# Kernel tuning notes

Measured on AMD Instinct MI355X. Metric: run time of the kernel, lower is better.

Reference implementation:

```python
import jax, jax.numpy as jnp
import numpy as np

B = 16384
C = 512          # mean candidate count per sample
T = B * C        # total flat logits length (static)


def _seg_ce(logits, counts, gt, valid, B):
    """Segmented cross-entropy over variable-length candidate sets.
    logits: [T] flat concatenated logits; counts: [B] segment lengths (sum == T);
    gt: [B] target index within each segment; valid: [B] bool mask.
    Returns (mean loss over valid samples, n_correct, n_valid)."""
    Ttot = logits.shape[0]
    offsets = jnp.cumsum(counts) - counts                       # [B] start of each segment
    seg = jnp.repeat(jnp.arange(B), counts, total_repeat_length=Ttot)  # [T] segment ids
    segmax = jax.ops.segment_max(logits, seg, num_segments=B)   # [B]
    ex = jnp.exp(logits - segmax[seg])
    Z = jax.ops.segment_sum(ex, seg, num_segments=B)            # [B]
    lse = jnp.log(Z) + segmax                                   # [B] logsumexp per segment
    # target logit: clamp position for safety; invalid rows are masked out anyway
    pos = offsets + jnp.clip(gt, 0, jnp.maximum(counts - 1, 0))
    ce = lse - logits[pos]                                      # [B]
    in_range = (gt >= 0) & (gt < counts)
    vmask = (counts > 0) & in_range & valid
    n_valid = vmask.sum()
    loss = jnp.where(vmask, ce, 0.0).sum() / jnp.maximum(n_valid, 1)
    # argmax within each segment (first occurrence, matching torch.argmax)
    local = jnp.arange(Ttot) - offsets[seg]
    is_max = logits == segmax[seg]
    arg = jax.ops.segment_min(jnp.where(is_max, local, Ttot), seg, num_segments=B)
    n_correct = (vmask & (arg == gt)).sum()
    return loss, n_correct, n_valid


def setup_inputs() -> dict:
    key = jax.random.key(0)
    ks = jax.random.split(key, 8)
    # counts alternate C+32 / C-32 so sum == B*C exactly (static T)
    counts = jnp.where(jnp.arange(B) % 2 == 0, C + 32, C - 32).astype(jnp.int32)
    sys_logits = jax.random.normal(ks[0], (T,), dtype=jnp.float32)
    bar_logits = jax.random.normal(ks[1], (T,), dtype=jnp.float32)
    gt_system_idx = jax.random.randint(ks[2], (B,), 0, C - 32).astype(jnp.int32)
    gt_bar_in_sys = jax.random.randint(ks[3], (B,), 0, C - 32).astype(jnp.int32)
    note_positions = jax.random.uniform(ks[4], (B,), dtype=jnp.float32)
    gt_note_position = jax.random.uniform(ks[5], (B,), dtype=jnp.float32)
    gt_valid = jax.random.bernoulli(ks[6], 0.97, (B,))
    return {
        'sys_logits': sys_logits, 'sys_counts': counts,
        'bar_logits': bar_logits, 'bar_counts': counts,
        'note_positions': note_positions,
        'gt_system_idx': gt_system_idx, 'gt_bar_in_sys': gt_bar_in_sys,
        'gt_note_position': gt_note_position, 'gt_valid': gt_valid,
        'log_var_sys': jnp.zeros((), jnp.float32),
        'log_var_bar': jnp.zeros((), jnp.float32),
        'log_var_note': jnp.zeros((), jnp.float32),
    }


def reference(sys_logits, sys_counts, bar_logits, bar_counts, note_positions,
              gt_system_idx, gt_bar_in_sys, gt_note_position, gt_valid,
              log_var_sys, log_var_bar, log_var_note):
    Bn = gt_system_idx.shape[0]
    sys_loss, sys_correct, n_valid = _seg_ce(sys_logits, sys_counts, gt_system_idx, gt_valid, Bn)
    bar_loss, bar_correct, n_valid_bar = _seg_ce(bar_logits, bar_counts, gt_bar_in_sys, gt_valid, Bn)
    # note position MSE over valid samples (bar_valid == gt_valid here)
    m = gt_valid
    nsel = m.sum()
    sq = jnp.where(m, (note_positions - gt_note_position) ** 2, 0.0)
    note_loss = jnp.where(nsel > 0, sq.sum() / jnp.maximum(nsel, 1), 0.0)
    prec_sys = jnp.exp(-log_var_sys)
    prec_bar = jnp.exp(-log_var_bar)
    prec_note = jnp.exp(-log_var_note)
    loss = (0.5 * prec_sys * sys_loss + 0.5 * log_var_sys
            + 0.5 * prec_bar * bar_loss + 0.5 * log_var_bar
            + 0.5 * prec_note * note_loss + 0.5 * log_var_note)
    sys_acc = sys_correct / jnp.maximum(n_valid, 1)
    bar_acc = bar_correct / jnp.maximum(n_valid_bar, 1)
    return (loss, sys_loss, bar_loss, note_loss, sys_acc, bar_acc,
            prec_sys, prec_bar, prec_note)
```

## Files before the change

### kernel.cpp

```cpp
#include <hip/hip_runtime.h>
#include <math.h>

#define SCAN_BLOCKS 256
#define NOTE_SQ   256
#define NOTE_CNT  512
#define DESC_BASE 1024

__device__ __forceinline__ bool is_valid(const void* gv, int flag, int i) {
  if (flag == 0) return ((const int*)gv)[i] != 0;
  if (flag == 1) return ((const unsigned char*)gv)[i] != 0;
  return ((const float*)gv)[i] != 0.0f;
}

__global__ __launch_bounds__(256)
void uwl_scan_desc(const int* __restrict__ c_sys, const int* __restrict__ c_bar,
                   const int* __restrict__ gt_sys, const int* __restrict__ gt_bar,
                   const void* __restrict__ gv,
                   const float* __restrict__ npos, const float* __restrict__ gnp,
                   int B, int* __restrict__ wsI, float* __restrict__ wsF) {
  const int blk = blockIdx.x;
  const int tid = threadIdx.x;
  const int lane = tid & 63;
  const int wid = tid >> 6;
  __shared__ int s_flag;
  __shared__ int sS[4], sB[4];
  const int chunk = (B + SCAN_BLOCKS - 1) / SCAN_BLOCKS;
  const int start0 = blk * chunk;
  const int start = (start0 < B) ? start0 : B;
  const int end = (start0 + chunk < B) ? start0 + chunk : B;
  if (tid < 64) {
    int nw = B / 4; if (nw > 64) nw = 64; if (nw < 1) nw = 1;
    const unsigned int x = (tid < nw) ? ((const unsigned int*)gv)[tid] : 0u;
    const bool all01 = __all(x <= 1u);
    const bool allf = __all(x == 0u || x == 0x3F800000u);
    if (tid == 0) s_flag = all01 ? 0 : (allf ? 2 : 1);
  }
  if (blk == 0) {
    if (tid >= 1 && tid <= 8) wsI[tid * 16] = 0;
    if (tid == 9) wsI[144] = 0;
  }
  int bs = 0, bb = 0;
  {
    const int s4 = start >> 2;
    const int4* cs4 = (const int4*)c_sys;
    const int4* cb4 = (const int4*)c_bar;
    for (int j = tid; j < s4; j += 256) {
      const int4 a = cs4[j]; bs += a.x + a.y + a.z + a.w;
      const int4 b = cb4[j]; bb += b.x + b.y + b.z + b.w;
    }
    if (tid < (start & 3)) {
      bs += c_sys[(s4 << 2) + tid];
      bb += c_bar[(s4 << 2) + tid];
    }
  }
#pragma unroll
  for (int d = 1; d < 64; d <<= 1) {
    bs += __shfl_xor(bs, d, 64);
    bb += __shfl_xor(bb, d, 64);
  }
  if (lane == 0) { sS[wid] = bs; sB[wid] = bb; }
  __syncthreads();
  const int flag = s_flag;
  if (wid == 0) {
    int carry1 = sS[0] + sS[1] + sS[2] + sS[3];
    int carry2 = sB[0] + sB[1] + sB[2] + sB[3];
    int4* descS = (int4*)(wsI + DESC_BASE);
    int4* descB = descS + B;
    for (int base = start; base < end; base += 64) {
      const int idx = base + lane;
      const bool ok = idx < end;
      const int x1 = ok ? c_sys[idx] : 0;
      const int x2 = ok ? c_bar[idx] : 0;
      int o1 = x1, o2 = x2;
#pragma unroll
      for (int d = 1; d < 64; d <<= 1) {
        const int v1 = __shfl_up(o1, d, 64);
        const int v2 = __shfl_up(o2, d, 64);
        if (lane >= d) { o1 += v1; o2 += v2; }
      }
      if (ok) {
        const int g1 = gt_sys[idx], g2 = gt_bar[idx];
        const bool v = is_valid(gv, flag, idx);
        descS[idx] = make_int4(carry1 + o1 - x1, x1, g1,
                               (x1 > 0 && g1 >= 0 && g1 < x1 && v) ? 1 : 0);
        descB[idx] = make_int4(carry2 + o2 - x2, x2, g2,
                               (x2 > 0 && g2 >= 0 && g2 < x2 && v) ? 1 : 0);
      }
      carry1 += __shfl(o1, 63, 64);
      carry2 += __shfl(o2, 63, 64);
    }
  } else if (wid == 1) {
    float sq = 0.f; int cnt = 0;
    for (int i = start + lane; i < end; i += 64) {
      if (is_valid(gv, flag, i)) {
        const float d = npos[i] - gnp[i];
        sq += d * d; cnt += 1;
      }
    }
#pragma unroll
    for (int d = 1; d < 64; d <<= 1) {
      sq += __shfl_xor(sq, d, 64);
      cnt += __shfl_xor(cnt, d, 64);
    }
    if (lane == 0) {
      wsF[NOTE_SQ + blk] = sq;
      wsI[NOTE_CNT + blk] = cnt;
    }
  }
}

__global__ __launch_bounds__(256)
void uwl_ce_kernel(const float* __restrict__ sys_lg, const float* __restrict__ bar_lg,
                   int B, int* __restrict__ wsI, float* __restrict__ wsF) {
  const int lane = threadIdx.x & 63;
  const int wid = threadIdx.x >> 6;
  const int wstep = (int)(gridDim.x << 2);
  for (int wave0 = (int)(blockIdx.x << 2) + wid; wave0 < 2 * B; wave0 += wstep) {
    const int wave = __builtin_amdgcn_readfirstlane(wave0);
    const int4 d4 = ((const int4*)(wsI + DESC_BASE))[wave];
    const float* lg = (wave < B) ? sys_lg : bar_lg;
    const int off_i = d4.x, count = d4.y, gt = d4.z, vld = d4.w;
    const long long off = off_i;

    float m = -INFINITY;
    float s = 0.f;
    float tl = 0.f;
    const bool regpath = (count >= 4) && (count <= 576) &&
                         ((off_i & 3) == 0) && ((count & 3) == 0);
    if (regpath) {
      const float4* p = (const float4*)(lg + off);
      const int emax = (count >> 2) - 1;
      float vals[8];
#pragma unroll
      for (int k = 0; k < 2; ++k) {
        const int e4 = (k << 6) + lane;
        const int ec = (e4 > emax) ? emax : e4;
        const float4 v = p[ec];
        const bool live = (e4 <= emax);
        vals[4 * k]     = live ? v.x : -INFINITY;
        vals[4 * k + 1] = live ? v.y : -INFINITY;
        vals[4 * k + 2] = live ? v.z : -INFINITY;
        vals[4 * k + 3] = live ? v.w : -INFINITY;
      }
      const int ti = 512 + lane;
      const int tic = (ti < count) ? ti : (count - 1);
      const float tvr = lg[off + tic];
      const float tv = (ti < count) ? tvr : -INFINITY;
#pragma unroll
      for (int k = 0; k < 8; ++k) m = fmaxf(m, vals[k]);
      m = fmaxf(m, tv);
#pragma unroll
      for (int k = 0; k < 8; ++k) s += __expf(vals[k]);
      s += __expf(tv);
      const int gts = vld ? gt : 0;
      float pick;
      int srclane;
      if (gts < 512) {
        const int q = ((gts >> 8) << 2) | (gts & 3);
        pick = vals[0];
#pragma unroll
        for (int i = 1; i < 8; ++i) pick = (i == q) ? vals[i] : pick;
        srclane = (gts >> 2) & 63;
      } else {
        pick = tv;
        srclane = gts - 512;
      }
      tl = __shfl(pick, srclane, 64);
    } else {
      for (int i = lane; i < count; i += 64) {
        const float v = lg[off + i];
        m = fmaxf(m, v);
        s += __expf(v);
      }
      if (vld) {
        const float t0 = (lane == 0) ? lg[off + gt] : 0.f;
        tl = __shfl(t0, 0, 64);
      }
    }
#pragma unroll
    for (int d = 1; d < 64; d <<= 1) {
      s += __shfl_xor(s, d, 64);
      m = fmaxf(m, __shfl_xor(m, d, 64));
    }
    if (lane == 0) {
      float ce = 0.f, code = 0.f;
      if (vld) {
        ce = __logf(s) - tl;
        code = (tl == m) ? 3.f : 1.f;
      }
      ((float2*)(wsF + DESC_BASE + 8 * B))[wave] = make_float2(ce, code);
    }
  }
}

__global__ __launch_bounds__(256)
void uwl_reduce_kernel(const float* __restrict__ lvs_p, const float* __restrict__ lvb_p,
                       const float* __restrict__ lvn_p,
                       int B, int* wsI, float* wsF, float* __restrict__ out) {
  const float4* pw4 = (const float4*)(wsF + DESC_BASE + 8 * B);
  float ces = 0.f, ceb = 0.f;
  int nvs = 0, cs = 0, nvb = 0, cb = 0;
  const int stride = gridDim.x * blockDim.x;
  for (int j = blockIdx.x * blockDim.x + threadIdx.x; j < B; j += stride) {
    const float4 v = pw4[j];
    const int e0 = 2 * j, e1 = 2 * j + 1;
    const int c0 = (int)v.y, c1 = (int)v.w;
    if (e0 < B) { ces += v.x; nvs += c0 & 1; cs += c0 >> 1; }
    else        { ceb += v.x; nvb += c0 & 1; cb += c0 >> 1; }
    if (e1 < B) { ces += v.z; nvs += c1 & 1; cs += c1 >> 1; }
    else        { ceb += v.z; nvb += c1 & 1; cb += c1 >> 1; }
  }
  float sq = 0.f; int cnt = 0;
  if (blockIdx.x == 0 && threadIdx.x < SCAN_BLOCKS) {
    sq = wsF[NOTE_SQ + threadIdx.x];
    cnt = wsI[NOTE_CNT + threadIdx.x];
  }
#pragma unroll
  for (int d = 1; d < 64; d <<= 1) {
    ces += __shfl_xor(ces, d, 64);
    ceb += __shfl_xor(ceb, d, 64);
    nvs += __shfl_xor(nvs, d, 64);
    cs  += __shfl_xor(cs,  d, 64);
    nvb += __shfl_xor(nvb, d, 64);
    cb  += __shfl_xor(cb,  d, 64);
    sq  += __shfl_xor(sq,  d, 64);
    cnt += __shfl_xor(cnt, d, 64);
  }
  if ((threadIdx.x & 63) == 0) {
    atomicAdd(&wsI[16], nvs);
    atomicAdd(&wsI[32], cs);
    atomicAdd(&wsF[48], ces);
    atomicAdd(&wsI[64], nvb);
    atomicAdd(&wsI[80], cb);
    atomicAdd(&wsF[96], ceb);
    atomicAdd(&wsI[112], cnt);
    atomicAdd(&wsF[128], sq);
  }
  __syncthreads();
  if (threadIdx.x == 0) {
    __threadfence();
    const int t = atomicAdd(&wsI[144], 1);
    if (t == (int)gridDim.x - 1) {
      __threadfence();
      const int fnvs = atomicAdd(&wsI[16], 0);
      const int fcs  = atomicAdd(&wsI[32], 0);
      const int fnvb = atomicAdd(&wsI[64], 0);
      const int fcb  = atomicAdd(&wsI[80], 0);
      const int fnn  = atomicAdd(&wsI[112], 0);
      const float fces = atomicAdd(&wsF[48], 0.f);
      const float fceb = atomicAdd(&wsF[96], 0.f);
      const float fsq  = atomicAdd(&wsF[128], 0.f);
      const float sys_loss = fces / (float)(fnvs > 1 ? fnvs : 1);
      const float bar_loss = fceb / (float)(fnvb > 1 ? fnvb : 1);
      const float note_loss = (fnn > 0) ? fsq / (float)fnn : 0.f;
      const float lvs = lvs_p[0], lvb = lvb_p[0], lvn = lvn_p[0];
      const float ps = expf(-lvs), pb = expf(-lvb), pn = expf(-lvn);
      out[0] = 0.5f * (ps * sys_loss + lvs + pb * bar_loss + lvb + pn * note_loss + lvn);
      out[1] = sys_loss;
      out[2] = bar_loss;
      out[3] = note_loss;
      out[4] = (float)fcs / (float)(fnvs > 1 ? fnvs : 1);
      out[5] = (float)fcb / (float)(fnvb > 1 ? fnvb : 1);
      out[6] = ps;
      out[7] = pb;
      out[8] = pn;
    }
  }
}

extern "C" void kernel_launch(void* const* d_in, const int* in_sizes, int n_in,
                              void* d_out, int out_size, void* d_ws, size_t ws_size,
                              hipStream_t stream) {
  const float* sys_lg = (const float*)d_in[0];
  const int*   c_sys  = (const int*)d_in[1];
  const float* bar_lg = (const float*)d_in[2];
  const int*   c_bar  = (const int*)d_in[3];
  const float* npos   = (const float*)d_in[4];
  const int*   gt_sys = (const int*)d_in[5];
  const int*   gt_bar = (const int*)d_in[6];
  const float* gnp    = (const float*)d_in[7];
  const void*  gv     = d_in[8];
  const float* lvs    = (const float*)d_in[9];
  const float* lvb    = (const float*)d_in[10];
  const float* lvn    = (const float*)d_in[11];
  const int B = in_sizes[1];

  int*   wsI = (int*)d_ws;
  float* wsF = (float*)d_ws;

  uwl_scan_desc<<<SCAN_BLOCKS, 256, 0, stream>>>(c_sys, c_bar, gt_sys, gt_bar, gv,
                                                 npos, gnp, B, wsI, wsF);

  const long long nwaveslots = ((long long)(2 * B) + 3) / 4;
  int nblocks = (int)((nwaveslots < 2048) ? nwaveslots : 2048);
  if (nblocks < 1) nblocks = 1;
  uwl_ce_kernel<<<nblocks, 256, 0, stream>>>(sys_lg, bar_lg, B, wsI, wsF);

  uwl_reduce_kernel<<<64, 256, 0, stream>>>(lvs, lvb, lvn, B, wsI, wsF, (float*)d_out);
}
```

Measured before the change: 131.6 us.

## Fuse descriptor scan and segment CE into one kernel with per-block prefix recompute

Merges the count-scan/descriptor kernel and the cross-entropy kernel into one kernel. Each block now owns 16 segments, recomputes its global offset by summing all preceding counts, and keeps the descriptors in shared memory. Per-block partial sums go to the workspace and a single-block final kernel reduces them, replacing the atomic last-block reduction. Valid and correct counts are packed into one int using 16-bit fields. This removes a launch and the descriptor round trip through global memory, but every block redundantly re-reads the count prefix, which adds a lot of L2 traffic. The 16-bit packing also limits the batch size.

```diff
diff --git a/kernel.cpp b/kernel.cpp
--- a/kernel.cpp
+++ b/kernel.cpp
@@ -1,10 +1,7 @@
 #include <hip/hip_runtime.h>
 #include <math.h>
 
-#define SCAN_BLOCKS 256
-#define NOTE_SQ   256
-#define NOTE_CNT  512
-#define DESC_BASE 1024
+#define SEG_PER_BLOCK 16
 
 __device__ __forceinline__ bool is_valid(const void* gv, int flag, int i) {
   if (flag == 0) return ((const int*)gv)[i] != 0;
@@ -13,21 +10,24 @@
 }
 
 __global__ __launch_bounds__(256)
-void uwl_scan_desc(const int* __restrict__ c_sys, const int* __restrict__ c_bar,
-                   const int* __restrict__ gt_sys, const int* __restrict__ gt_bar,
-                   const void* __restrict__ gv,
-                   const float* __restrict__ npos, const float* __restrict__ gnp,
-                   int B, int* __restrict__ wsI, float* __restrict__ wsF) {
-  const int blk = blockIdx.x;
+void uwl_fused(const float* __restrict__ sys_lg, const float* __restrict__ bar_lg,
+               const int* __restrict__ c_sys, const int* __restrict__ c_bar,
+               const int* __restrict__ gt_sys, const int* __restrict__ gt_bar,
+               const void* __restrict__ gv,
+               const float* __restrict__ npos, const float* __restrict__ gnp,
+               int B, int NB, int* __restrict__ wsI, float* __restrict__ wsF) {
+  const int b = blockIdx.x;
   const int tid = threadIdx.x;
   const int lane = tid & 63;
   const int wid = tid >> 6;
+  const int g0 = b * SEG_PER_BLOCK;
   __shared__ int s_flag;
-  __shared__ int sS[4], sB[4];
-  const int chunk = (B + SCAN_BLOCKS - 1) / SCAN_BLOCKS;
-  const int start0 = blk * chunk;
-  const int start = (start0 < B) ? start0 : B;
-  const int end = (start0 + chunk < B) ? start0 + chunk : B;
+  __shared__ int sOff[SEG_PER_BLOCK], sCnt[SEG_PER_BLOCK];
+  __shared__ int sGt[SEG_PER_BLOCK], sVld[SEG_PER_BLOCK];
+  __shared__ int sB1[4], sB2[4];
+  __shared__ float sCe[4], sCb[4];
+  __shared__ int sCo[4], sCob[4];
+
   if (tid < 64) {
     int nw = B / 4; if (nw > 64) nw = 64; if (nw < 1) nw = 1;
     const unsigned int x = (tid < nw) ? ((const unsigned int*)gv)[tid] : 0u;
@@ -35,63 +35,62 @@
     const bool allf = __all(x == 0u || x == 0x3F800000u);
     if (tid == 0) s_flag = all01 ? 0 : (allf ? 2 : 1);
   }
-  if (blk == 0) {
-    if (tid >= 1 && tid <= 8) wsI[tid * 16] = 0;
-    if (tid == 9) wsI[144] = 0;
-  }
+
+  const int e1 = (g0 < B) ? g0 : 0;
+  int e2 = g0 - B; if (e2 < 0) e2 = 0; if (e2 > B) e2 = B;
   int bs = 0, bb = 0;
   {
-    const int s4 = start >> 2;
-    const int4* cs4 = (const int4*)c_sys;
-    const int4* cb4 = (const int4*)c_bar;
-    for (int j = tid; j < s4; j += 256) {
-      const int4 a = cs4[j]; bs += a.x + a.y + a.z + a.w;
-      const int4 b = cb4[j]; bb += b.x + b.y + b.z + b.w;
-    }
-    if (tid < (start & 3)) {
-      bs += c_sys[(s4 << 2) + tid];
-      bb += c_bar[(s4 << 2) + tid];
-    }
+    const int s4 = e1 >> 2;
+    const int4* c4 = (const int4*)c_sys;
+    for (int j = tid; j < s4; j += 256) { const int4 a = c4[j]; bs += a.x + a.y + a.z + a.w; }
+    if (tid < (e1 & 3)) bs += c_sys[(s4 << 2) + tid];
+  }
+  {
+    const int s4 = e2 >> 2;
+    const int4* c4 = (const int4*)c_bar;
+    for (int j = tid; j < s4; j += 256) { const int4 a = c4[j]; bb += a.x + a.y + a.z + a.w; }
+    if (tid < (e2 & 3)) bb += c_bar[(s4 << 2) + tid];
   }
 #pragma unroll
   for (int d = 1; d < 64; d <<= 1) {
     bs += __shfl_xor(bs, d, 64);
     bb += __shfl_xor(bb, d, 64);
   }
-  if (lane == 0) { sS[wid] = bs; sB[wid] = bb; }
+  if (lane == 0) { sB1[wid] = bs; sB2[wid] = bb; }
   __syncthreads();
   const int flag = s_flag;
+
   if (wid == 0) {
-    int carry1 = sS[0] + sS[1] + sS[2] + sS[3];
-    int carry2 = sB[0] + sB[1] + sB[2] + sB[3];
-    int4* descS = (int4*)(wsI + DESC_BASE);
-    int4* descB = descS + B;
-    for (int base = start; base < end; base += 64) {
-      const int idx = base + lane;
-      const bool ok = idx < end;
-      const int x1 = ok ? c_sys[idx] : 0;
-      const int x2 = ok ? c_bar[idx] : 0;
-      int o1 = x1, o2 = x2;
-#pragma unroll
-      for (int d = 1; d < 64; d <<= 1) {
-        const int v1 = __shfl_up(o1, d, 64);
-        const int v2 = __shfl_up(o2, d, 64);
-        if (lane >= d) { o1 += v1; o2 += v2; }
-      }
-      if (ok) {
-        const int g1 = gt_sys[idx], g2 = gt_bar[idx];
-        const bool v = is_valid(gv, flag, idx);
-        descS[idx] = make_int4(carry1 + o1 - x1, x1, g1,
-                               (x1 > 0 && g1 >= 0 && g1 < x1 && v) ? 1 : 0);
-        descB[idx] = make_int4(carry2 + o2 - x2, x2, g2,
-                               (x2 > 0 && g2 >= 0 && g2 < x2 && v) ? 1 : 0);
-      }
-      carry1 += __shfl(o1, 63, 64);
-      carry2 += __shfl(o2, 63, 64);
+    const int base1 = sB1[0] + sB1[1] + sB1[2] + sB1[3];
+    const int base2 = sB2[0] + sB2[1] + sB2[2] + sB2[3];
+    const int g = g0 + lane;
+    const bool okseg = (lane < SEG_PER_BLOCK) && (g < 2 * B);
+    const bool isSys = g < B;
+    const int smp = isSys ? g : g - B;
+    const int cnt = okseg ? (isSys ? c_sys[g] : c_bar[smp]) : 0;
+    int inc = cnt;
+#pragma unroll
+    for (int d = 1; d < SEG_PER_BLOCK; d <<= 1) {
+      const int v = __shfl_up(inc, d, 64);
+      if (lane >= d) inc += v;
+    }
+    int S = 0;
+    const int tb = B - g0;
+    if (tb > 0 && tb < SEG_PER_BLOCK) S = __shfl(inc, tb - 1, 64);
+    if (okseg) {
+      const int gt = isSys ? gt_sys[g] : gt_bar[smp];
+      const bool v = is_valid(gv, flag, smp);
+      sOff[lane] = (isSys ? base1 : base2 - S) + inc - cnt;
+      sCnt[lane] = cnt;
+      sGt[lane] = gt;
+      sVld[lane] = (cnt > 0 && gt >= 0 && gt < cnt && v) ? 1 : 0;
     }
   } else if (wid == 1) {
+    const int ns = (B + NB - 1) / NB;
+    const int n0 = b * ns;
+    const int n1 = (n0 + ns < B) ? n0 + ns : B;
     float sq = 0.f; int cnt = 0;
-    for (int i = start + lane; i < end; i += 64) {
+    for (int i = n0 + lane; i < n1; i += 64) {
       if (is_valid(gv, flag, i)) {
         const float d = npos[i] - gnp[i];
         sq += d * d; cnt += 1;
@@ -102,24 +101,19 @@
       sq += __shfl_xor(sq, d, 64);
       cnt += __shfl_xor(cnt, d, 64);
     }
-    if (lane == 0) {
-      wsF[NOTE_SQ + blk] = sq;
-      wsI[NOTE_CNT + blk] = cnt;
-    }
-  }
-}
-
-__global__ __launch_bounds__(256)
-void uwl_ce_kernel(const float* __restrict__ sys_lg, const float* __restrict__ bar_lg,
-                   int B, int* __restrict__ wsI, float* __restrict__ wsF) {
-  const int lane = threadIdx.x & 63;
-  const int wid = threadIdx.x >> 6;
-  const int wstep = (int)(gridDim.x << 2);
-  for (int wave0 = (int)(blockIdx.x << 2) + wid; wave0 < 2 * B; wave0 += wstep) {
-    const int wave = __builtin_amdgcn_readfirstlane(wave0);
-    const int4 d4 = ((const int4*)(wsI + DESC_BASE))[wave];
-    const float* lg = (wave < B) ? sys_lg : bar_lg;
-    const int off_i = d4.x, count = d4.y, gt = d4.z, vld = d4.w;
+    if (lane == 0) { wsF[256 + 2 * NB + b] = sq; wsI[256 + 5 * NB + b] = cnt; }
+  }
+  __syncthreads();
+
+  float ces = 0.f, ceb = 0.f;
+  int cods = 0, codb = 0;
+#pragma unroll 1
+  for (int k = 0; k < 4; ++k) {
+    const int t = (wid << 2) | k;
+    const int g = g0 + t;
+    if (g >= 2 * B) break;
+    const int off_i = sOff[t], count = sCnt[t], gt = sGt[t], vld = sVld[t];
+    const float* lg = (g < B) ? sys_lg : bar_lg;
     const long long off = off_i;
 
     float m = -INFINITY;
@@ -132,25 +126,25 @@
       const int emax = (count >> 2) - 1;
       float vals[8];
 #pragma unroll
-      for (int k = 0; k < 2; ++k) {
-        const int e4 = (k << 6) + lane;
+      for (int kk = 0; kk < 2; ++kk) {
+        const int e4 = (kk << 6) + lane;
         const int ec = (e4 > emax) ? emax : e4;
         const float4 v = p[ec];
         const bool live = (e4 <= emax);
-        vals[4 * k]     = live ? v.x : -INFINITY;
-        vals[4 * k + 1] = live ? v.y : -INFINITY;
-        vals[4 * k + 2] = live ? v.z : -INFINITY;
-        vals[4 * k + 3] = live ? v.w : -INFINITY;
+        vals[4 * kk]     = live ? v.x : -INFINITY;
+        vals[4 * kk + 1] = live ? v.y : -INFINITY;
+        vals[4 * kk + 2] = live ? v.z : -INFINITY;
+        vals[4 * kk + 3] = live ? v.w : -INFINITY;
       }
       const int ti = 512 + lane;
       const int tic = (ti < count) ? ti : (count - 1);
       const float tvr = lg[off + tic];
       const float tv = (ti < count) ? tvr : -INFINITY;
 #pragma unroll
-      for (int k = 0; k < 8; ++k) m = fmaxf(m, vals[k]);
+      for (int kk = 0; kk < 8; ++kk) m = fmaxf(m, vals[kk]);
       m = fmaxf(m, tv);
 #pragma unroll
-      for (int k = 0; k < 8; ++k) s += __expf(vals[k]);
+      for (int kk = 0; kk < 8; ++kk) s += __expf(vals[kk]);
       s += __expf(tv);
       const int gts = vld ? gt : 0;
       float pick;
@@ -182,89 +176,78 @@
       s += __shfl_xor(s, d, 64);
       m = fmaxf(m, __shfl_xor(m, d, 64));
     }
-    if (lane == 0) {
-      float ce = 0.f, code = 0.f;
-      if (vld) {
-        ce = __logf(s) - tl;
-        code = (tl == m) ? 3.f : 1.f;
-      }
-      ((float2*)(wsF + DESC_BASE + 8 * B))[wave] = make_float2(ce, code);
-    }
+    if (vld) {
+      const float ce = __logf(s) - tl;
+      const int code = 1 + ((tl == m) ? 65536 : 0);
+      if (g < B) { ces += ce; cods += code; }
+      else       { ceb += ce; codb += code; }
+    }
+  }
+  if (lane == 0) { sCe[wid] = ces; sCb[wid] = ceb; sCo[wid] = cods; sCob[wid] = codb; }
+  __syncthreads();
+  if (tid == 0) {
+    wsF[256 + b]          = sCe[0] + sCe[1] + sCe[2] + sCe[3];
+    wsF[256 + NB + b]     = sCb[0] + sCb[1] + sCb[2] + sCb[3];
+    wsI[256 + 3 * NB + b] = sCo[0] + sCo[1] + sCo[2] + sCo[3];
+    wsI[256 + 4 * NB + b] = sCob[0] + sCob[1] + sCob[2] + sCob[3];
   }
 }
 
 __global__ __launch_bounds__(256)
-void uwl_reduce_kernel(const float* __restrict__ lvs_p, const float* __restrict__ lvb_p,
-                       const float* __restrict__ lvn_p,
-                       int B, int* wsI, float* wsF, float* __restrict__ out) {
-  const float4* pw4 = (const float4*)(wsF + DESC_BASE + 8 * B);
-  float ces = 0.f, ceb = 0.f;
-  int nvs = 0, cs = 0, nvb = 0, cb = 0;
-  const int stride = gridDim.x * blockDim.x;
-  for (int j = blockIdx.x * blockDim.x + threadIdx.x; j < B; j += stride) {
-    const float4 v = pw4[j];
-    const int e0 = 2 * j, e1 = 2 * j + 1;
-    const int c0 = (int)v.y, c1 = (int)v.w;
-    if (e0 < B) { ces += v.x; nvs += c0 & 1; cs += c0 >> 1; }
-    else        { ceb += v.x; nvb += c0 & 1; cb += c0 >> 1; }
-    if (e1 < B) { ces += v.z; nvs += c1 & 1; cs += c1 >> 1; }
-    else        { ceb += v.z; nvb += c1 & 1; cb += c1 >> 1; }
-  }
-  float sq = 0.f; int cnt = 0;
-  if (blockIdx.x == 0 && threadIdx.x < SCAN_BLOCKS) {
-    sq = wsF[NOTE_SQ + threadIdx.x];
-    cnt = wsI[NOTE_CNT + threadIdx.x];
+void uwl_final(const float* __restrict__ lvs_p, const float* __restrict__ lvb_p,
+               const float* __restrict__ lvn_p,
+               int B, int NB, const int* __restrict__ wsI,
+               const float* __restrict__ wsF, float* __restrict__ out) {
+  const int tid = threadIdx.x;
+  const int lane = tid & 63;
+  const int wid = tid >> 6;
+  float ces = 0.f, ceb = 0.f, sq = 0.f;
+  int cods = 0, codb = 0, cnt = 0;
+  for (int i = tid; i < NB; i += 256) {
+    ces  += wsF[256 + i];
+    ceb  += wsF[256 + NB + i];
+    sq   += wsF[256 + 2 * NB + i];
+    cods += wsI[256 + 3 * NB + i];
+    codb += wsI[256 + 4 * NB + i];
+    cnt  += wsI[256 + 5 * NB + i];
   }
 #pragma unroll
   for (int d = 1; d < 64; d <<= 1) {
-    ces += __shfl_xor(ces, d, 64);
-    ceb += __shfl_xor(ceb, d, 64);
-    nvs += __shfl_xor(nvs, d, 64);
-    cs  += __shfl_xor(cs,  d, 64);
-    nvb += __shfl_xor(nvb, d, 64);
-    cb  += __shfl_xor(cb,  d, 64);
-    sq  += __shfl_xor(sq,  d, 64);
-    cnt += __shfl_xor(cnt, d, 64);
-  }
-  if ((threadIdx.x & 63) == 0) {
-    atomicAdd(&wsI[16], nvs);
-    atomicAdd(&wsI[32], cs);
-    atomicAdd(&wsF[48], ces);
-    atomicAdd(&wsI[64], nvb);
-    atomicAdd(&wsI[80], cb);
-    atomicAdd(&wsF[96], ceb);
-    atomicAdd(&wsI[112], cnt);
-    atomicAdd(&wsF[128], sq);
-  }
-  __syncthreads();
-  if (threadIdx.x == 0) {
-    __threadfence();
-    const int t = atomicAdd(&wsI[144], 1);
-    if (t == (int)gridDim.x - 1) {
-      __threadfence();
-      const int fnvs = atomicAdd(&wsI[16], 0);
-      const int fcs  = atomicAdd(&wsI[32], 0);
-      const int fnvb = atomicAdd(&wsI[64], 0);
-      const int fcb  = atomicAdd(&wsI[80], 0);
-      const int fnn  = atomicAdd(&wsI[112], 0);
-      const float fces = atomicAdd(&wsF[48], 0.f);
-      const float fceb = atomicAdd(&wsF[96], 0.f);
-      const float fsq  = atomicAdd(&wsF[128], 0.f);
-      const float sys_loss = fces / (float)(fnvs > 1 ? fnvs : 1);
-      const float bar_loss = fceb / (float)(fnvb > 1 ? fnvb : 1);
-      const float note_loss = (fnn > 0) ? fsq / (float)fnn : 0.f;
-      const float lvs = lvs_p[0], lvb = lvb_p[0], lvn = lvn_p[0];
-      const float ps = expf(-lvs), pb = expf(-lvb), pn = expf(-lvn);
-      out[0] = 0.5f * (ps * sys_loss + lvs + pb * bar_loss + lvb + pn * note_loss + lvn);
-      out[1] = sys_loss;
-      out[2] = bar_loss;
-      out[3] = note_loss;
-      out[4] = (float)fcs / (float)(fnvs > 1 ? fnvs : 1);
-      out[5] = (float)fcb / (float)(fnvb > 1 ? fnvb : 1);
-      out[6] = ps;
-      out[7] = pb;
-      out[8] = pn;
-    }
+    ces  += __shfl_xor(ces, d, 64);
+    ceb  += __shfl_xor(ceb, d, 64);
+    sq   += __shfl_xor(sq, d, 64);
+    cods += __shfl_xor(cods, d, 64);
+    codb += __shfl_xor(codb, d, 64);
+    cnt  += __shfl_xor(cnt, d, 64);
+  }
+  __shared__ float f0[4], f1[4], f2[4];
+  __shared__ int i0[4], i1[4], i2[4];
+  if (lane == 0) { f0[wid] = ces; f1[wid] = ceb; f2[wid] = sq;
+                   i0[wid] = cods; i1[wid] = codb; i2[wid] = cnt; }
+  __syncthreads();
+  if (tid == 0) {
+    const float fces = f0[0] + f0[1] + f0[2] + f0[3];
+    const float fceb = f1[0] + f1[1] + f1[2] + f1[3];
+    const float fsq  = f2[0] + f2[1] + f2[2] + f2[3];
+    const int fs = i0[0] + i0[1] + i0[2] + i0[3];
+    const int fb = i1[0] + i1[1] + i1[2] + i1[3];
+    const int fnn = i2[0] + i2[1] + i2[2] + i2[3];
+    const int fnvs = fs & 0xFFFF, fcs = fs >> 16;
+    const int fnvb = fb & 0xFFFF, fcb = fb >> 16;
+    const float sys_loss = fces / (float)(fnvs > 1 ? fnvs : 1);
+    const float bar_loss = fceb / (float)(fnvb > 1 ? fnvb : 1);
+    const float note_loss = (fnn > 0) ? fsq / (float)fnn : 0.f;
+    const float lvs = lvs_p[0], lvb = lvb_p[0], lvn = lvn_p[0];
+    const float ps = expf(-lvs), pb = expf(-lvb), pn = expf(-lvn);
+    out[0] = 0.5f * (ps * sys_loss + lvs + pb * bar_loss + lvb + pn * note_loss + lvn);
+    out[1] = sys_loss;
+    out[2] = bar_loss;
+    out[3] = note_loss;
+    out[4] = (float)fcs / (float)(fnvs > 1 ? fnvs : 1);
+    out[5] = (float)fcb / (float)(fnvb > 1 ? fnvb : 1);
+    out[6] = ps;
+    out[7] = pb;
+    out[8] = pn;
   }
 }
 
@@ -288,13 +271,10 @@
   int*   wsI = (int*)d_ws;
   float* wsF = (float*)d_ws;
 
-  uwl_scan_desc<<<SCAN_BLOCKS, 256, 0, stream>>>(c_sys, c_bar, gt_sys, gt_bar, gv,
-                                                 npos, gnp, B, wsI, wsF);
-
-  const long long nwaveslots = ((long long)(2 * B) + 3) / 4;
-  int nblocks = (int)((nwaveslots < 2048) ? nwaveslots : 2048);
-  if (nblocks < 1) nblocks = 1;
-  uwl_ce_kernel<<<nblocks, 256, 0, stream>>>(sys_lg, bar_lg, B, wsI, wsF);
-
-  uwl_reduce_kernel<<<64, 256, 0, stream>>>(lvs, lvb, lvn, B, wsI, wsF, (float*)d_out);
-}
+  int NB = (2 * B + SEG_PER_BLOCK - 1) / SEG_PER_BLOCK;
+  if (NB < 1) NB = 1;
+
+  uwl_fused<<<NB, 256, 0, stream>>>(sys_lg, bar_lg, c_sys, c_bar, gt_sys, gt_bar,
+                                    gv, npos, gnp, B, NB, wsI, wsF);
+  uwl_final<<<1, 256, 0, stream>>>(lvs, lvb, lvn, B, NB, wsI, wsF, (float*)d_out);
+}
```

Result: faster. 125.2 us (-4.9%).
